# Optimization experiments

Measured on AMD Instinct MI355X. Metric: run time of the kernel, lower is better.

## Reference

```python
import jax, jax.numpy as jnp
import numpy as np

NUM_HEADS = 16
SRC_FACTS = 4


def setup_inputs() -> dict:
    key = jax.random.key(0)
    k1, k2, k3, k4, k5 = jax.random.split(key, 5)
    B, S, H, Dh = 16, 512, NUM_HEADS, 64  # B = batch(4) * src_facts(4)
    D = H * Dh  # d_model = 1024
    pre_q = jax.random.normal(k1, (B, S, H, Dh), dtype=jnp.float32)
    pre_v = jax.random.normal(k2, (B, S, H, Dh), dtype=jnp.float32)
    pre_k = jax.random.normal(k3, (B, S, H, Dh), dtype=jnp.float32)
    attn_mask = jax.random.randint(k4, (B, S, S), 0, 2).astype(jnp.int32)
    output_weights = jax.random.normal(k5, (D, D), dtype=jnp.float32) / np.float32(np.sqrt(D))
    return {
        "pre_q": pre_q,
        "pre_v": pre_v,
        "pre_k": pre_k,
        "attn_mask": attn_mask,
        "output_weights": output_weights,
        "out_seq_len": 512,
        "d_model": 1024,
    }


def reference(pre_q, pre_v, pre_k, attn_mask, output_weights, out_seq_len, d_model):
    B, Sq, H, Dh = pre_q.shape
    # Original: K.sqrt(cast(d_model) // num_heads) -> sqrt(head_dim)
    scale = jnp.sqrt(jnp.float32(float(d_model) // H))
    mask = attn_mask.astype(jnp.float32)[:, None]  # (B, 1, q, k) broadcast over heads
    # scores: (B, H, q, k)
    scores = jnp.einsum("bqhd,bkhd->bhqk", pre_q, pre_k) / scale
    # multiplicative pre-mask + additive -1e9 on masked slots
    scores = scores * mask + (1.0 - mask) * jnp.float32(-1e9)
    # softmax then multiplicative post-mask
    attn = jax.nn.softmax(scores, axis=-1) * mask
    heads = jnp.einsum("bhqk,bkhd->bqhd", attn, pre_v)  # (B, q, H, Dh)
    out = heads.reshape(B, Sq, H * Dh) @ output_weights  # (B, q, d_model)
    return out.reshape(-1, SRC_FACTS, out_seq_len, d_model)
```

## Files before the change

### kernel.cpp

```cpp
#include <hip/hip_runtime.h>
#include <hip/hip_bf16.h>


typedef __bf16 bf16;
typedef bf16 bf16x8 __attribute__((ext_vector_type(8)));
typedef bf16 bf16x4 __attribute__((ext_vector_type(4)));
typedef float floatx4 __attribute__((ext_vector_type(4)));
typedef unsigned short ushort8 __attribute__((ext_vector_type(8)));
typedef unsigned long long u64;

#define MFMA32(A, B, C) __builtin_amdgcn_mfma_f32_16x16x32_bf16((A), (B), (C), 0, 0, 0)

namespace {
constexpr int S   = 512;
constexpr int H   = 16;
constexpr int Dh  = 64;
constexpr int D   = 1024;
constexpr int LDT = 72;
constexpr size_t QN = (size_t)16 * S * H * Dh;
constexpr size_t WN = (size_t)D * D;
}

__global__ __launch_bounds__(256)
void prep_kernel(const float* __restrict__ Kf, const float* __restrict__ Vf,
                 const float* __restrict__ Wf, const int* __restrict__ Mg,
                 bf16* __restrict__ Kc, bf16* __restrict__ Vt,
                 bf16* __restrict__ Wt, u64* __restrict__ MB)
{
    __shared__ bf16 Ts[64 * LDT];
    const int blk = blockIdx.x, tid = threadIdx.x;

    if (blk < 4096) {
        const int i = blk * 256 + tid;
        const float* fs = Kf + (size_t)i * 8;
        bf16x8 v;
#pragma unroll
        for (int j = 0; j < 8; ++j) v[j] = (bf16)fs[j];
        *(bf16x8*)(Kc + (size_t)i * 8) = v;
    } else if (blk < 6144) {
        const int bk2 = blk - 4096;
        const int bh  = bk2 >> 3, st = bk2 & 7;
        const int b   = bh >> 4, h = bh & 15;
        const int r   = tid >> 2, c = (tid & 3) * 16;
        const float* src = Vf + ((size_t)((b * S + st * 64 + r) * H + h)) * Dh + c;
#pragma unroll
        for (int i = 0; i < 16; ++i)
            Ts[(c + i) * LDT + r] = (bf16)src[i];
        __syncthreads();
        bf16* dst = Vt + ((size_t)bh * 64 + r) * S + st * 64 + c;
        *(ushort8*)dst       = *(const ushort8*)&Ts[r * LDT + c];
        *(ushort8*)(dst + 8) = *(const ushort8*)&Ts[r * LDT + c + 8];
    } else if (blk < 6400) {
        const int bk2 = blk - 6144;
        const int nb  = bk2 & 15, kb = bk2 >> 4;
        const int r   = tid >> 2, c = (tid & 3) * 16;
        const float* src = Wf + (size_t)(kb * 64 + r) * D + nb * 64 + c;
#pragma unroll
        for (int i = 0; i < 16; ++i)
            Ts[(c + i) * LDT + r] = (bf16)src[i];
        __syncthreads();
        bf16* dst = Wt + (size_t)(nb * 64 + r) * D + kb * 64 + c;
        *(ushort8*)dst       = *(const ushort8*)&Ts[r * LDT + c];
        *(ushort8*)(dst + 8) = *(const ushort8*)&Ts[r * LDT + c + 8];
    } else {
        const int bk2  = blk - 6400;
        const int lane = tid & 63;
        const int idx4 = bk2 * 4 + (tid >> 6);
        const int row  = idx4 >> 1;
        const int half = idx4 & 1;
#pragma unroll
        for (int r = 0; r < 4; ++r) {
            int mv = Mg[(size_t)row * 512 + half * 256 + r * 64 + lane];
            u64 bm = __ballot(mv != 0);
            if (lane == 0) MB[(size_t)row * 8 + half * 4 + r] = bm;
        }
    }
}

__global__ __launch_bounds__(256, 4)
void attn_kernel(const float* __restrict__ Qg, const bf16* __restrict__ Kc,
                 const bf16* __restrict__ Vtg, const u64* __restrict__ MB,
                 bf16* __restrict__ heads)
{
    __shared__ bf16 Ks[64 * LDT];
    __shared__ bf16 Vt[64 * LDT];

    const int tid  = threadIdx.x;
    const int lane = tid & 63;
    const int wave = tid >> 6;
    const int l15  = lane & 15;
    const int quad = lane >> 4;

    const int blk = blockIdx.x;
    const int h   = blk & 15;
    const int qt  = (blk >> 4) & 7;
    const int b   = blk >> 7;
    const int qw  = qt * 64 + wave * 16;

    bf16x8 aq0, aq1;
    {
        const float* qb = Qg + ((size_t)((b * S + qw + l15) * H + h)) * Dh + quad * 8;
        floatx4 f0 = *(const floatx4*)qb;
        floatx4 f1 = *(const floatx4*)(qb + 4);
        floatx4 f2 = *(const floatx4*)(qb + 32);
        floatx4 f3 = *(const floatx4*)(qb + 36);
#pragma unroll
        for (int j = 0; j < 4; ++j) {
            aq0[j]     = (bf16)(f0[j] * 0.125f);
            aq0[j + 4] = (bf16)(f1[j] * 0.125f);
            aq1[j]     = (bf16)(f2[j] * 0.125f);
            aq1[j + 4] = (bf16)(f3[j] * 0.125f);
        }
    }

    float rsum = 0.f;
    floatx4 O[4];
#pragma unroll
    for (int i = 0; i < 4; ++i) O[i] = floatx4{0.f, 0.f, 0.f, 0.f};

    const u64* mbrow = MB + ((size_t)b * S + qw + l15) * 8;
    const bf16* vplane = Vtg + (size_t)(b * 16 + h) * 64 * S;

    const int sr = tid >> 2, sc_ = (tid & 3) * 16;
    const int kperm = ((sr >> 5) << 5) | (((sr & 15) >> 2) << 3)
                    | (((sr >> 4) & 1) << 2) | (sr & 3);

    for (int kt = 0; kt < 8; ++kt) {
        const int kb = kt * 64;
        const bf16* ksrc = Kc + ((size_t)((b * S + kb + kperm) * H + h)) * Dh + sc_;
        const bf16* vsrc = vplane + (size_t)sr * S + kb + sc_;
        ushort8 k0 = *(const ushort8*)ksrc;
        ushort8 k1 = *(const ushort8*)(ksrc + 8);
        ushort8 v0 = *(const ushort8*)vsrc;
        ushort8 v1 = *(const ushort8*)(vsrc + 8);
        u64 m64 = mbrow[kt];

        __syncthreads();
        *(ushort8*)&Ks[sr * LDT + sc_]     = k0;
        *(ushort8*)&Ks[sr * LDT + sc_ + 8] = k1;
        *(ushort8*)&Vt[sr * LDT + sc_]     = v0;
        *(ushort8*)&Vt[sr * LDT + sc_ + 8] = v1;
        __syncthreads();

        bf16x8 pB[2];
#pragma unroll
        for (int mt = 0; mt < 4; ++mt) {
            bf16x8 ak0 = *(const bf16x8*)&Ks[(mt * 16 + l15) * LDT + quad * 8];
            bf16x8 ak1 = *(const bf16x8*)&Ks[(mt * 16 + l15) * LDT + quad * 8 + 32];
            floatx4 acc = floatx4{0.f, 0.f, 0.f, 0.f};
            acc = MFMA32(ak0, aq0, acc);
            acc = MFMA32(ak1, aq1, acc);
            const int block = mt >> 1, tile = mt & 1;
            const int kbase = block * 32 + quad * 8 + tile * 4;
#pragma unroll
            for (int reg = 0; reg < 4; ++reg) {
                unsigned bit = (unsigned)(m64 >> (kbase + reg)) & 1u;
                float e = __expf(acc[reg]);
                float p = bit ? e : 0.f;
                rsum += p;
                pB[block][tile * 4 + reg] = (bf16)p;
            }
        }

#pragma unroll
        for (int block = 0; block < 2; ++block) {
#pragma unroll
            for (int mt = 0; mt < 4; ++mt) {
                bf16x8 av = *(const bf16x8*)&Vt[(mt * 16 + l15) * LDT + block * 32 + quad * 8];
                O[mt] = MFMA32(av, pB[block], O[mt]);
            }
        }
    }

    rsum += __shfl_xor(rsum, 16, 64);
    rsum += __shfl_xor(rsum, 32, 64);
    const float inv = (rsum > 0.f) ? (1.f / rsum) : 0.f;

    bf16* hrow = heads + ((size_t)((b * S + qw + l15) * H + h)) * Dh;
#pragma unroll
    for (int mt = 0; mt < 4; ++mt) {
        bf16x4 h4;
#pragma unroll
        for (int reg = 0; reg < 4; ++reg) h4[reg] = (bf16)(O[mt][reg] * inv);
        *(bf16x4*)&hrow[mt * 16 + quad * 4] = h4;
    }
}

__global__ __launch_bounds__(256)
void proj_kernel(const bf16* __restrict__ A, const bf16* __restrict__ Wt,
                 float* __restrict__ out)
{
    __shared__ bf16 As[128 * LDT];
    __shared__ bf16 Ws[128 * LDT];

    const int tid  = threadIdx.x;
    const int lane = tid & 63;
    const int wave = tid >> 6;
    const int l15  = lane & 15;
    const int quad = lane >> 4;

    const int nb = blockIdx.x & 7;
    const int mb = blockIdx.x >> 3;
    const int mbase = mb * 128, nbase = nb * 128;
    const int wm = (wave & 1) * 64, wn = (wave >> 1) * 64;

    const int pr = tid >> 1, pc = (tid & 1) * 32;

    floatx4 O[4][4];
#pragma unroll
    for (int mt = 0; mt < 4; ++mt)
#pragma unroll
        for (int nt = 0; nt < 4; ++nt) O[mt][nt] = floatx4{0.f, 0.f, 0.f, 0.f};

    for (int kt = 0; kt < 16; ++kt) {
        const int kb = kt * 64;
        const bf16* asrc = A  + (size_t)(mbase + pr) * D + kb + pc;
        const bf16* wsrc = Wt + (size_t)(nbase + pr) * D + kb + pc;
        ushort8 a0 = *(const ushort8*)asrc;
        ushort8 a1 = *(const ushort8*)(asrc + 8);
        ushort8 a2 = *(const ushort8*)(asrc + 16);
        ushort8 a3 = *(const ushort8*)(asrc + 24);
        ushort8 w0 = *(const ushort8*)wsrc;
        ushort8 w1 = *(const ushort8*)(wsrc + 8);
        ushort8 w2 = *(const ushort8*)(wsrc + 16);
        ushort8 w3 = *(const ushort8*)(wsrc + 24);

        __syncthreads();
        *(ushort8*)&As[pr * LDT + pc]      = a0;
        *(ushort8*)&As[pr * LDT + pc + 8]  = a1;
        *(ushort8*)&As[pr * LDT + pc + 16] = a2;
        *(ushort8*)&As[pr * LDT + pc + 24] = a3;
        *(ushort8*)&Ws[pr * LDT + pc]      = w0;
        *(ushort8*)&Ws[pr * LDT + pc + 8]  = w1;
        *(ushort8*)&Ws[pr * LDT + pc + 16] = w2;
        *(ushort8*)&Ws[pr * LDT + pc + 24] = w3;
        __syncthreads();

        bf16x8 fa[4][2];
#pragma unroll
        for (int mt = 0; mt < 4; ++mt) {
            fa[mt][0] = *(const bf16x8*)&As[(wm + mt * 16 + l15) * LDT + quad * 8];
            fa[mt][1] = *(const bf16x8*)&As[(wm + mt * 16 + l15) * LDT + quad * 8 + 32];
        }
#pragma unroll
        for (int nt = 0; nt < 4; ++nt) {
            bf16x8 fb0 = *(const bf16x8*)&Ws[(wn + nt * 16 + l15) * LDT + quad * 8];
            bf16x8 fb1 = *(const bf16x8*)&Ws[(wn + nt * 16 + l15) * LDT + quad * 8 + 32];
#pragma unroll
            for (int mt = 0; mt < 4; ++mt) {
                O[mt][nt] = MFMA32(fa[mt][0], fb0, O[mt][nt]);
                O[mt][nt] = MFMA32(fa[mt][1], fb1, O[mt][nt]);
            }
        }
    }

#pragma unroll
    for (int mt = 0; mt < 4; ++mt) {
#pragma unroll
        for (int nt = 0; nt < 4; ++nt) {
#pragma unroll
            for (int reg = 0; reg < 4; ++reg) {
                const int m = mbase + wm + mt * 16 + quad * 4 + reg;
                const int n = nbase + wn + nt * 16 + l15;
                out[(size_t)m * D + n] = O[mt][nt][reg];
            }
        }
    }
}

extern "C" void kernel_launch(void* const* d_in, const int* in_sizes, int n_in,
                              void* d_out, int out_size, void* d_ws, size_t ws_size,
                              hipStream_t stream)
{
    const float* pre_q = (const float*)d_in[0];
    const float* pre_v = (const float*)d_in[1];
    const float* pre_k = (const float*)d_in[2];
    const int*   mask  = (const int*)d_in[3];
    const float* Wg    = (const float*)d_in[4];
    float* out = (float*)d_out;

    bf16* Kc    = (bf16*)d_ws;
    bf16* Vt    = Kc + QN;
    bf16* Wt    = Vt + QN;
    bf16* heads = Wt + WN;
    u64*  MB    = (u64*)(heads + QN);

    prep_kernel<<<10496, 256, 0, stream>>>(pre_k, pre_v, Wg, mask, Kc, Vt, Wt, MB);
    attn_kernel<<<2048, 256, 0, stream>>>(pre_q, Kc, Vt, MB, heads);
    proj_kernel<<<512, 256, 0, stream>>>(heads, Wt, out);
}
```

Before: 215.9 us.

## Prefetch next K/V tile into registers and use exp2 with bitmask select

Software-pipelines the attention loop: global loads of the next K/V tile and mask word are issued right after the LDS barrier, so they overlap the current tile's MFMA and softmax work. The log2(e) factor is folded into the Q scale so the exponential becomes a raw exp2 instruction. The mask test becomes a sign-extended bitfield AND in place of a 64-bit shift and select. The prefetch keeps more live registers, which could lower occupancy.

```diff
diff --git a/kernel.cpp b/kernel.cpp
--- a/kernel.cpp
+++ b/kernel.cpp
@@ -19,6 +19,22 @@
 constexpr int LDT = 72;
 constexpr size_t QN = (size_t)16 * S * H * Dh;
 constexpr size_t WN = (size_t)D * D;
+}
+
+__device__ __forceinline__ float fexp2(float x) {
+#if defined(__HIP_DEVICE_COMPILE__) && __has_builtin(__builtin_amdgcn_exp2f)
+    return __builtin_amdgcn_exp2f(x);
+#else
+    return exp2f(x);
+#endif
+}
+
+__device__ __forceinline__ int sbfe1(unsigned bits, int bit) {
+#if defined(__HIP_DEVICE_COMPILE__) && __has_builtin(__builtin_amdgcn_sbfe)
+    return __builtin_amdgcn_sbfe((int)bits, (unsigned)bit, 1u);
+#else
+    return ((int)(bits << (31 - bit))) >> 31;
+#endif
 }
 
 __global__ __launch_bounds__(256)
@@ -97,6 +113,7 @@
     const int b   = blk >> 7;
     const int qw  = qt * 64 + wave * 16;
 
+    constexpr float QSCL = 0.125f * 1.44269504088896340736f;
     bf16x8 aq0, aq1;
     {
         const float* qb = Qg + ((size_t)((b * S + qw + l15) * H + h)) * Dh + quad * 8;
@@ -106,10 +123,10 @@
         floatx4 f3 = *(const floatx4*)(qb + 36);
 #pragma unroll
         for (int j = 0; j < 4; ++j) {
-            aq0[j]     = (bf16)(f0[j] * 0.125f);
-            aq0[j + 4] = (bf16)(f1[j] * 0.125f);
-            aq1[j]     = (bf16)(f2[j] * 0.125f);
-            aq1[j + 4] = (bf16)(f3[j] * 0.125f);
+            aq0[j]     = (bf16)(f0[j] * QSCL);
+            aq0[j + 4] = (bf16)(f1[j] * QSCL);
+            aq1[j]     = (bf16)(f2[j] * QSCL);
+            aq1[j + 4] = (bf16)(f3[j] * QSCL);
         }
     }
 
@@ -125,22 +142,36 @@
     const int kperm = ((sr >> 5) << 5) | (((sr & 15) >> 2) << 3)
                     | (((sr >> 4) & 1) << 2) | (sr & 3);
 
+    const bf16* ksrc0 = Kc + ((size_t)((b * S + kperm) * H + h)) * Dh + sc_;
+    const bf16* vsrc0 = vplane + (size_t)sr * S + sc_;
+
+    ushort8 k0 = *(const ushort8*)ksrc0;
+    ushort8 k1 = *(const ushort8*)(ksrc0 + 8);
+    ushort8 v0 = *(const ushort8*)vsrc0;
+    ushort8 v1 = *(const ushort8*)(vsrc0 + 8);
+    u64 m64 = mbrow[0];
+
     for (int kt = 0; kt < 8; ++kt) {
-        const int kb = kt * 64;
-        const bf16* ksrc = Kc + ((size_t)((b * S + kb + kperm) * H + h)) * Dh + sc_;
-        const bf16* vsrc = vplane + (size_t)sr * S + kb + sc_;
-        ushort8 k0 = *(const ushort8*)ksrc;
-        ushort8 k1 = *(const ushort8*)(ksrc + 8);
-        ushort8 v0 = *(const ushort8*)vsrc;
-        ushort8 v1 = *(const ushort8*)(vsrc + 8);
-        u64 m64 = mbrow[kt];
-
         __syncthreads();
         *(ushort8*)&Ks[sr * LDT + sc_]     = k0;
         *(ushort8*)&Ks[sr * LDT + sc_ + 8] = k1;
         *(ushort8*)&Vt[sr * LDT + sc_]     = v0;
         *(ushort8*)&Vt[sr * LDT + sc_ + 8] = v1;
-        __syncthreads();
+        const u64 mcur = m64;
+        __syncthreads();
+
+        if (kt < 7) {
+            const bf16* ks = ksrc0 + (size_t)(kt + 1) * 64 * H * Dh;
+            const bf16* vs = vsrc0 + (kt + 1) * 64;
+            k0 = *(const ushort8*)ks;
+            k1 = *(const ushort8*)(ks + 8);
+            v0 = *(const ushort8*)vs;
+            v1 = *(const ushort8*)(vs + 8);
+            m64 = mbrow[kt + 1];
+        }
+
+        const unsigned qlo = (unsigned)(mcur >> (quad * 8));
+        const unsigned qhi = (unsigned)(mcur >> (quad * 8 + 32));
 
         bf16x8 pB[2];
 #pragma unroll
@@ -151,12 +182,12 @@
             acc = MFMA32(ak0, aq0, acc);
             acc = MFMA32(ak1, aq1, acc);
             const int block = mt >> 1, tile = mt & 1;
-            const int kbase = block * 32 + quad * 8 + tile * 4;
+            const unsigned bits = (block ? qhi : qlo) >> (tile * 4);
 #pragma unroll
             for (int reg = 0; reg < 4; ++reg) {
-                unsigned bit = (unsigned)(m64 >> (kbase + reg)) & 1u;
-                float e = __expf(acc[reg]);
-                float p = bit ? e : 0.f;
+                float e = fexp2(acc[reg]);
+                int sx = sbfe1(bits, reg);
+                float p = __uint_as_float(__float_as_uint(e) & (unsigned)sx);
                 rsum += p;
                 pB[block][tile * 4 + reg] = (bf16)p;
             }
```

Result: slower. 242.8 us (+12.4%).
